# Optimization experiments

Measured on AMD Instinct MI355X. Metric: run time of the kernel, lower is better.

The kernel has to match this reference:

```python
import jax, jax.numpy as jnp
import numpy as np


def setup_inputs() -> dict:
    key = jax.random.key(0)
    k1, k2 = jax.random.split(key)
    B, S, H = 8, 2048, 1024
    decoder_state_t = jax.random.normal(k1, (B, H), dtype=jnp.float32)
    encoder_outputs = jax.random.normal(k2, (B, S, H), dtype=jnp.float32)
    return {"decoder_state_t": decoder_state_t, "encoder_outputs": encoder_outputs}


def reference(decoder_state_t, encoder_outputs):
    # decoder_state_t: (B, H); encoder_outputs: (B, S, H)
    B, S, H = encoder_outputs.shape
    # state_trans = tile(decoder_state_t.unsqueeze(1), (S, 1)) -> (B, S, H), all rows identical
    state_trans = jnp.broadcast_to(decoder_state_t[:, None, :], (B, S, H))
    # multip = state_trans @ encoder_outputs^T -> (B, S, S)
    multip = jnp.einsum("bih,bjh->bij", state_trans, encoder_outputs)
    # sum over last dim -> (B, S); every row i has the same value (degenerate math, kept faithful)
    attention_scores = jax.nn.softmax(jnp.sum(multip, axis=-1), axis=-1)
    # context = sum_s scores[b,s] * encoder_outputs[b,s,:] -> (B, H)
    context = jnp.einsum("bs,bsh->bh", attention_scores, encoder_outputs)
    return (context, attention_scores)
```

## Files before the change

### kernel.cpp

```cpp
#include <hip/hip_runtime.h>

#define BB 8
#define SS 2048
#define HH 1024
#define NCHUNK 64
#define CHUNK (SS / NCHUNK)
#define NBLK (BB * NCHUNK)

typedef float vf4 __attribute__((ext_vector_type(4)));

__global__ void __launch_bounds__(256, 4)
att_partial_kernel(const float* __restrict__ enc, float* __restrict__ partial) {
    const int g = blockIdx.x;
    const int b = g >> 6;
    const int c = g & (NCHUNK - 1);
    const int t = threadIdx.x;
    const vf4* p =
        (const vf4*)(enc + ((size_t)b * SS + (size_t)c * CHUNK) * HH) + t;

    vf4 acc = (vf4)(0.f);
    #pragma unroll
    for (int pass = 0; pass < 4; ++pass) {
        vf4 v[8];
        #pragma unroll
        for (int s = 0; s < 8; ++s)
            v[s] = __builtin_nontemporal_load(p + (size_t)(pass * 8 + s) * (HH / 4));
        #pragma unroll
        for (int st = 4; st > 0; st >>= 1) {
            #pragma unroll
            for (int s = 0; s < st; ++s) v[s] += v[s + st];
        }
        acc += v[0];
    }
    *((vf4*)(partial + (size_t)g * HH) + t) = acc;
}

__global__ void __launch_bounds__(256)
att_finalize_kernel(const float* __restrict__ partial, float* __restrict__ out) {
    const int blk = blockIdx.x;
    const int b = blk >> 4;
    const int hbase = (blk & 15) * 64;
    const int t = threadIdx.x;
    const int hl = t & 63;
    const int cq = t >> 6;

    const float* p =
        partial + ((size_t)(b * NCHUNK + cq * 16)) * HH + hbase + hl;
    float acc = 0.f;
    #pragma unroll
    for (int c = 0; c < 16; ++c) acc += p[(size_t)c * HH];

    const float inv = 1.0f / SS;
    if (t >= 64 && t < 192) {
        out[BB * HH + blk * 128 + (t - 64)] = inv;
    }

    __shared__ float lds[4][64];
    lds[cq][hl] = acc;
    __syncthreads();
    if (t < 64) {
        float s = lds[0][t] + lds[1][t] + lds[2][t] + lds[3][t];
        out[b * HH + hbase + t] = s * inv;
    }
}

__global__ void __launch_bounds__(256)
att_direct_kernel(const float* __restrict__ enc, float* __restrict__ out) {
    int tid = blockIdx.x * blockDim.x + threadIdx.x;
    if (tid < BB * HH) {
        int b = tid >> 10;
        int h = tid & (HH - 1);
        const float* p = enc + (size_t)b * SS * HH + h;
        float acc = 0.f;
        for (int s = 0; s < SS; ++s) acc += p[(size_t)s * HH];
        out[tid] = acc * (1.0f / SS);
    } else if (tid < BB * HH + BB * SS) {
        out[tid] = 1.0f / SS;
    }
}

extern "C" void kernel_launch(void* const* d_in, const int* in_sizes, int n_in,
                              void* d_out, int out_size, void* d_ws, size_t ws_size,
                              hipStream_t stream) {
    const float* enc = (const float*)d_in[1];
    float* out = (float*)d_out;

    const size_t part_bytes = (size_t)NBLK * HH * sizeof(float);
    if (d_ws != nullptr && ws_size >= part_bytes) {
        float* partial = (float*)d_ws;
        att_partial_kernel<<<NBLK, 256, 0, stream>>>(enc, partial);
        att_finalize_kernel<<<128, 256, 0, stream>>>(partial, out);
    } else {
        const int total_out = BB * HH + BB * SS;
        att_direct_kernel<<<(total_out + 255) / 256, 256, 0, stream>>>(enc, out);
    }
}
```

Before: 16.17 us.

## Fuse partial and finalize into a single column-owning reduction kernel

Replaces the two-kernel scheme (per-row-chunk partial sums written to workspace, then a finalize pass) with one kernel. In it, each block owns a 16-column slice of one batch and reduces it over all 2048 rows, finishing with an LDS tree reduction. This removes the second launch and the workspace round trip. The cost is that each wavefront now reads 64-byte fragments strided by a full row, instead of contiguous 4KB rows. On this bandwidth-bound read of 64MB, that access pattern may lower DRAM/L2 efficiency.

```diff
diff --git a/kernel.cpp b/kernel.cpp
--- a/kernel.cpp
+++ b/kernel.cpp
@@ -3,28 +3,32 @@
 #define BB 8
 #define SS 2048
 #define HH 1024
-#define NCHUNK 64
-#define CHUNK (SS / NCHUNK)
-#define NBLK (BB * NCHUNK)
+#define NSLICE 64
+#define NBLK (BB * NSLICE)
+#define SCORES_PER_BLK ((BB * SS) / NBLK)
 
 typedef float vf4 __attribute__((ext_vector_type(4)));
 
 __global__ void __launch_bounds__(256, 4)
-att_partial_kernel(const float* __restrict__ enc, float* __restrict__ partial) {
+att_colown_kernel(const float* __restrict__ enc, float* __restrict__ out) {
     const int g = blockIdx.x;
     const int b = g >> 6;
-    const int c = g & (NCHUNK - 1);
+    const int slice = g & (NSLICE - 1);
     const int t = threadIdx.x;
-    const vf4* p =
-        (const vf4*)(enc + ((size_t)b * SS + (size_t)c * CHUNK) * HH) + t;
+    const int c4 = t & 3;
+    const int rg = t >> 2;
+
+    const vf4* p = (const vf4*)(enc + (size_t)b * SS * HH + slice * 16) + c4;
 
     vf4 acc = (vf4)(0.f);
     #pragma unroll
     for (int pass = 0; pass < 4; ++pass) {
         vf4 v[8];
         #pragma unroll
-        for (int s = 0; s < 8; ++s)
-            v[s] = __builtin_nontemporal_load(p + (size_t)(pass * 8 + s) * (HH / 4));
+        for (int s = 0; s < 8; ++s) {
+            int r = rg + (pass * 8 + s) * 64;
+            v[s] = __builtin_nontemporal_load(p + (size_t)r * (HH / 4));
+        }
         #pragma unroll
         for (int st = 4; st > 0; st >>= 1) {
             #pragma unroll
@@ -32,35 +36,23 @@
         }
         acc += v[0];
     }
-    *((vf4*)(partial + (size_t)g * HH) + t) = acc;
-}
-
-__global__ void __launch_bounds__(256)
-att_finalize_kernel(const float* __restrict__ partial, float* __restrict__ out) {
-    const int blk = blockIdx.x;
-    const int b = blk >> 4;
-    const int hbase = (blk & 15) * 64;
-    const int t = threadIdx.x;
-    const int hl = t & 63;
-    const int cq = t >> 6;
-
-    const float* p =
-        partial + ((size_t)(b * NCHUNK + cq * 16)) * HH + hbase + hl;
-    float acc = 0.f;
-    #pragma unroll
-    for (int c = 0; c < 16; ++c) acc += p[(size_t)c * HH];
 
     const float inv = 1.0f / SS;
-    if (t >= 64 && t < 192) {
-        out[BB * HH + blk * 128 + (t - 64)] = inv;
+    if (t >= 192 && t < 192 + SCORES_PER_BLK) {
+        out[BB * HH + g * SCORES_PER_BLK + (t - 192)] = inv;
     }
 
-    __shared__ float lds[4][64];
-    lds[cq][hl] = acc;
+    __shared__ vf4 buf[256];
+    buf[t] = acc;
     __syncthreads();
-    if (t < 64) {
-        float s = lds[0][t] + lds[1][t] + lds[2][t] + lds[3][t];
-        out[b * HH + hbase + t] = s * inv;
+    #pragma unroll
+    for (int s = 128; s >= 4; s >>= 1) {
+        if (t < s) buf[t] += buf[t + s];
+        __syncthreads();
+    }
+    if (t < 4) {
+        vf4 r = buf[t] * inv;
+        *((vf4*)(out + (size_t)b * HH + slice * 16) + t) = r;
     }
 }
 
@@ -84,14 +76,6 @@
                               hipStream_t stream) {
     const float* enc = (const float*)d_in[1];
     float* out = (float*)d_out;
-
-    const size_t part_bytes = (size_t)NBLK * HH * sizeof(float);
-    if (d_ws != nullptr && ws_size >= part_bytes) {
-        float* partial = (float*)d_ws;
-        att_partial_kernel<<<NBLK, 256, 0, stream>>>(enc, partial);
-        att_finalize_kernel<<<128, 256, 0, stream>>>(partial, out);
-    } else {
-        const int total_out = BB * HH + BB * SS;
-        att_direct_kernel<<<(total_out + 255) / 256, 256, 0, stream>>>(enc, out);
-    }
+    (void)d_ws; (void)ws_size;
+    att_colown_kernel<<<NBLK, 256, 0, stream>>>(enc, out);
 }
```

Measured after the change: 28.48 us. 1.76x slower.
